# Optimization experiments

Hardware: AMD Instinct MI355X
Metric: run time of the kernel (lower is better)

Reference implementation:

```python
import jax, jax.numpy as jnp
import numpy as np

BN_EPS = 1e-5


def setup_inputs() -> dict:
    key = jax.random.key(0)
    ks = jax.random.split(key, 8)
    B, C, H, W = 8, 256, 64, 64
    Ci = 128
    x = jax.random.normal(ks[0], (B, C, H, W), dtype=jnp.float32)
    # 1x1 conv weights stored as [out, in] (kernel size 1 squeezed)
    sc = 1.0 / np.sqrt(C)
    g_w = jax.random.uniform(ks[1], (Ci, C), jnp.float32, -sc, sc)
    g_b = jax.random.uniform(ks[2], (Ci,), jnp.float32, -sc, sc)
    theta_w = jax.random.uniform(ks[3], (Ci, C), jnp.float32, -sc, sc)
    theta_b = jax.random.uniform(ks[4], (Ci,), jnp.float32, -sc, sc)
    phi_w = jax.random.uniform(ks[5], (Ci, C), jnp.float32, -sc, sc)
    phi_b = jax.random.uniform(ks[6], (Ci,), jnp.float32, -sc, sc)
    # W conv: normal(std=0.01) weight, zero bias (per _init_weights)
    W_w = 0.01 * jax.random.normal(ks[7], (C, Ci), dtype=jnp.float32)
    W_b = jnp.zeros((C,), dtype=jnp.float32)
    bn_gamma = jnp.ones((C,), dtype=jnp.float32)
    bn_beta = jnp.zeros((C,), dtype=jnp.float32)
    return {"x": x, "g_w": g_w, "g_b": g_b, "theta_w": theta_w, "theta_b": theta_b,
            "phi_w": phi_w, "phi_b": phi_b, "W_w": W_w, "W_b": W_b,
            "bn_gamma": bn_gamma, "bn_beta": bn_beta}


def reference(x, g_w, g_b, theta_w, theta_b, phi_w, phi_b, W_w, W_b, bn_gamma, bn_beta):
    B, C, H, W = x.shape
    xf = x.reshape(B, C, H * W)                                   # [B, C, N]
    # 1x1 convs == per-position channel GEMMs
    g_x = jnp.einsum('oc,bcn->bon', g_w, xf) + g_b[:, None]        # [B, Ci, N]
    th = jnp.einsum('oc,bcn->bon', theta_w, xf) + theta_b[:, None]
    ph = jnp.einsum('oc,bcn->bon', phi_w, xf) + phi_b[:, None]
    # theta^T phi : [B, N, N] dense attention scores
    f = jnp.einsum('bcn,bcm->bnm', th, ph)
    attn = jax.nn.softmax(f, axis=-1)
    # attention-weighted sum of g values -> [B, Ci, N]
    y = jnp.einsum('bnm,bcm->bcn', attn, g_x)
    # output 1x1 conv + BatchNorm2d (training-mode batch stats)
    wy = jnp.einsum('oc,bcn->bon', W_w, y) + W_b[:, None]          # [B, C, N]
    mean = jnp.mean(wy, axis=(0, 2), keepdims=True)
    var = jnp.var(wy, axis=(0, 2), keepdims=True)
    wy_bn = (wy - mean) * jax.lax.rsqrt(var + BN_EPS)
    wy_bn = wy_bn * bn_gamma[:, None] + bn_beta[:, None]
    z = wy_bn.reshape(B, C, H, W) + x
    return z
```

## Files before the change

### kernel.cpp

```cpp
#include <hip/hip_runtime.h>
#include <hip/hip_bf16.h>
#include <math.h>

#define B_   8
#define C_   256
#define CI_  128
#define N_   4096

typedef unsigned short ushort_t;
typedef unsigned int uint_t;
typedef __attribute__((ext_vector_type(8))) short short8;
typedef __attribute__((ext_vector_type(16))) float floatx16;
typedef __attribute__((ext_vector_type(2))) unsigned int uint2v;

#define OFF_W3B  0ull
#define OFF_B3   196608ull
#define OFF_WCB  198144ull
#define OFF_XT   263680ull
#define OFF_THT  17040896ull
#define OFF_PHT  25429504ull
#define OFF_G16  33818112ull
#define OFF_LP   42206720ull
#define OFF_YPB  42468864ull
#define OFF_WY   263680ull
#define OFF_ST   59246080ull

__device__ __forceinline__ ushort_t f2bf(float x) {
  union { float f; uint_t u; } c; c.f = x;
  return (ushort_t)((c.u + 0x7fffu + ((c.u >> 16) & 1u)) >> 16);
}
__device__ __forceinline__ uint_t pkbf(float a, float b) {
  __hip_bfloat162 h = __float22bfloat162_rn(float2{a, b});
  union { __hip_bfloat162 h; uint_t u; } c; c.h = h; return c.u;
}
__device__ __forceinline__ float bf_lo(uint_t u) {
  union { uint_t u; float f; } c; c.u = u << 16; return c.f;
}
__device__ __forceinline__ float bf_hi(uint_t u) {
  union { uint_t u; float f; } c; c.u = u & 0xffff0000u; return c.f;
}
__device__ __forceinline__ float fexp2(float x) {
  float r; asm("v_exp_f32 %0, %1\ns_nop 0" : "=v"(r) : "v"(x)); return r;
}
__device__ __forceinline__ void async_copy16(const void* g, void* l) {
  __builtin_amdgcn_global_load_lds(
      (const __attribute__((address_space(1))) unsigned int*)g,
      (__attribute__((address_space(3))) unsigned int*)l, 16, 0, 0);
}

__global__ __launch_bounds__(256) void pack_w(
    const float* __restrict__ g_w, const float* __restrict__ g_b,
    const float* __restrict__ th_w, const float* __restrict__ th_b,
    const float* __restrict__ ph_w, const float* __restrict__ ph_b,
    const float* __restrict__ W_w,
    ushort_t* __restrict__ W3b, float* __restrict__ b3,
    ushort_t* __restrict__ Wc)
{
  int bid = blockIdx.x;
  if (bid < 384) {
    int i = bid * 256 + threadIdx.x;
    int o = i >> 8;
    float v;
    if (o < 128)      v = g_w[i];
    else if (o < 256) v = th_w[i - 128*256];
    else              v = ph_w[i - 256*256];
    W3b[i] = f2bf(v);
    if ((i & 255) == 0)
      b3[o] = (o < 128) ? g_b[o] : (o < 256) ? th_b[o - 128] : ph_b[o - 256];
  } else {
    int j = (bid - 384) * 256 + threadIdx.x;
    Wc[j] = f2bf(W_w[j]);
  }
}

__global__ __launch_bounds__(256) void xcast(
    const float* __restrict__ x, ushort_t* __restrict__ xt)
{
  const int b = blockIdx.z, c0 = blockIdx.y * 64, n0 = blockIdx.x * 64;
  const int tid = threadIdx.x;
  __shared__ float xs[64][65];
  const int nq = (tid & 15) * 4, cr = tid >> 4;
  #pragma unroll
  for (int i = 0; i < 4; ++i) {
    float4 v = *(const float4*)&x[((size_t)b * C_ + c0 + cr + 16*i) * N_ + n0 + nq];
    xs[cr + 16*i][nq] = v.x; xs[cr + 16*i][nq+1] = v.y;
    xs[cr + 16*i][nq+2] = v.z; xs[cr + 16*i][nq+3] = v.w;
  }
  __syncthreads();
  const int n = tid >> 2, cs = (tid & 3) * 16;
  uint_t u[8];
  #pragma unroll
  for (int j = 0; j < 8; ++j)
    u[j] = pkbf(xs[cs + 2*j][n], xs[cs + 2*j + 1][n]);
  ushort_t* dst = &xt[((size_t)b * N_ + n0 + n) * C_ + c0 + cs];
  *(uint4*)dst       = make_uint4(u[0], u[1], u[2], u[3]);
  *(uint4*)(dst + 8) = make_uint4(u[4], u[5], u[6], u[7]);
}

__global__ __launch_bounds__(256, 2) void proj_all(
    const ushort_t* __restrict__ W3b, const float* __restrict__ b3,
    const ushort_t* __restrict__ xt, ushort_t* __restrict__ tht,
    ushort_t* __restrict__ pht, ushort_t* __restrict__ g16)
{
  const int b = blockIdx.z, nb = blockIdx.x, ot = blockIdx.y;
  const int gm = (ot == 2);
  const int o0 = gm ? 0 : (128 + ot * 128);
  const int tid = threadIdx.x, w = tid >> 6, lane = tid & 63;
  const int l31 = lane & 31, h = lane >> 5, xk = l31 & 7;
  __shared__ ushort_t ws_l[128 * 64];
  __shared__ ushort_t xs_l[128 * 64];
  const ushort_t* xb = xt + (size_t)b * N_ * C_;
  const int n0 = nb * 128;
  floatx16 acc[4];
  #pragma unroll
  for (int ct = 0; ct < 4; ++ct)
    #pragma unroll
    for (int r = 0; r < 16; ++r) acc[ct][r] = 0.f;

  const int gr = lane >> 3, gu = lane & 7;
  for (int k0 = 0; k0 < C_; k0 += 64) {
    __syncthreads();
    #pragma unroll
    for (int i = 0; i < 4; ++i) {
      int r = w*32 + i*8 + gr;
      async_copy16(&W3b[(size_t)(o0 + r) * C_ + k0 + ((gu ^ (r & 7)) * 8)],
                   &ws_l[(w*32 + i*8) * 64]);
      async_copy16(&xb[(size_t)(n0 + r) * C_ + k0 + ((gu ^ (r & 7)) * 8)],
                   &xs_l[(w*32 + i*8) * 64]);
    }
    __syncthreads();
    const ushort_t* bmat = gm ? ws_l : xs_l;
    const ushort_t* amat = gm ? xs_l : ws_l;
    #pragma unroll
    for (int kk = 0; kk < 4; ++kk) {
      int fc = ((2*kk + h) ^ xk) * 8;
      short8 bf = *(const short8*)&bmat[(w*32 + l31) * 64 + fc];
      #pragma unroll
      for (int ct = 0; ct < 4; ++ct) {
        short8 af = *(const short8*)&amat[(ct*32 + l31) * 64 + fc];
        acc[ct] = __builtin_amdgcn_mfma_f32_32x32x16_bf16(af, bf, acc[ct], 0, 0, 0);
      }
    }
  }

  if (gm) {
    float bv = b3[w*32 + l31];
    ushort_t* gp = g16 + ((size_t)b * CI_ + w*32 + l31) * N_;
    #pragma unroll
    for (int ct = 0; ct < 4; ++ct)
      #pragma unroll
      for (int rq = 0; rq < 4; ++rq) {
        uint2 d = make_uint2(pkbf(acc[ct][4*rq+0] + bv, acc[ct][4*rq+1] + bv),
                             pkbf(acc[ct][4*rq+2] + bv, acc[ct][4*rq+3] + bv));
        *(uint2*)&gp[n0 + ct*32 + 8*rq + 4*h] = d;
      }
  } else {
    ushort_t* tp = ((ot == 0) ? tht : pht) + ((size_t)b * N_ + n0 + w*32 + l31) * CI_;
    #pragma unroll
    for (int ct = 0; ct < 4; ++ct)
      #pragma unroll
      for (int rq = 0; rq < 4; ++rq) {
        float4 bv = *(const float4*)&b3[o0 + ct*32 + 8*rq + 4*h];
        uint2 d = make_uint2(pkbf(acc[ct][4*rq+0] + bv.x, acc[ct][4*rq+1] + bv.y),
                             pkbf(acc[ct][4*rq+2] + bv.z, acc[ct][4*rq+3] + bv.w));
        *(uint2*)&tp[ct*32 + 8*rq + 4*h] = d;
      }
  }
}

#define LOG2E_  1.442695041f
#define MBIAS_  (-28.85390082f)

__global__ __launch_bounds__(256, 3) void attn_mfma(
    const ushort_t* __restrict__ tht, const ushort_t* __restrict__ pht,
    const ushort_t* __restrict__ g16, ushort_t* __restrict__ yp,
    float* __restrict__ lp)
{
  const int b  = blockIdx.x & 7;
  const int ms = (blockIdx.x >> 3) & 1;
  const int qb = blockIdx.x >> 4;
  const int tid = threadIdx.x, w = tid >> 6, lane = tid & 63;
  const int l31 = lane & 31, h = lane >> 5, xk = l31 & 7;

  __shared__ ushort_t smem[24576];

  const int q0w = qb * 128 + w * 32;
  const int m_base = ms * 2048;

  const ushort_t* thb = tht + (size_t)b * N_ * CI_;
  const ushort_t* phb = pht + (size_t)b * N_ * CI_;
  const ushort_t* gbp = g16 + (size_t)b * CI_ * N_;

  short8 tf[8];
  #pragma unroll
  for (int kk = 0; kk < 8; ++kk)
    tf[kk] = *(const short8*)&thb[(size_t)(q0w + l31) * CI_ + kk*16 + h*8];

  floatx16 acc[4];
  #pragma unroll
  for (int ct = 0; ct < 4; ++ct)
    #pragma unroll
    for (int r = 0; r < 16; ++r) acc[ct][r] = 0.f;
  float lpart = 0.f;

  const int phr = lane >> 4, phu = lane & 15;
  const int gr  = lane >> 3, gu  = lane & 7;

  #define STAGE_PHS(m0v, bufv)                                                \
    {                                                                         \
      ushort_t* phs_ = smem + (bufv) * 8192;                                  \
      _Pragma("unroll")                                                       \
      for (int i = 0; i < 4; ++i) {                                           \
        int row = w*16 + i*4 + phr;                                           \
        async_copy16(&phb[(size_t)((m0v) + row) * CI_ + ((phu ^ (row & 7)) * 8)], \
                     &phs_[(w*16 + i*4) * 128]);                              \
      }                                                                       \
    }
  #define STAGE_GS(m0v)                                                       \
    {                                                                         \
      ushort_t* gs_ = smem + 16384;                                           \
      _Pragma("unroll")                                                       \
      for (int i = 0; i < 4; ++i) {                                           \
        int c = w*32 + i*8 + gr;                                              \
        async_copy16(&gbp[(size_t)c * N_ + (m0v) + ((gu ^ (c & 7)) * 8)],     \
                     &gs_[(w*32 + i*8) * 64]);                                \
      }                                                                       \
    }

  #define SMPV(sv, mtv)                                                       \
    {                                                                         \
      uint_t Aw[4], Bw[4];                                                    \
      float ls = 0.f;                                                         \
      _Pragma("unroll")                                                       \
      for (int rq = 0; rq < 4; ++rq) {                                        \
        float p0 = fexp2(fmaf(sv[4*rq+0], LOG2E_, MBIAS_));                   \
        float p1 = fexp2(fmaf(sv[4*rq+1], LOG2E_, MBIAS_));                   \
        float p2 = fexp2(fmaf(sv[4*rq+2], LOG2E_, MBIAS_));                   \
        float p3 = fexp2(fmaf(sv[4*rq+3], LOG2E_, MBIAS_));                   \
        ls += (p0 + p1) + (p2 + p3);                                          \
        Aw[rq] = pkbf(p0, p1);                                                \
        Bw[rq] = pkbf(p2, p3);                                                \
      }                                                                       \
      lpart += ls;                                                            \
      _Pragma("unroll")                                                       \
      for (int t = 0; t < 2; ++t) {                                           \
        uint2v ra = __builtin_amdgcn_permlane32_swap(Aw[2*t], Aw[2*t+1], false, false); \
        uint2v rb = __builtin_amdgcn_permlane32_swap(Bw[2*t], Bw[2*t+1], false, false); \
        union { uint_t u[4]; short8 s; } pk_;                                 \
        pk_.u[0] = ra.x; pk_.u[1] = rb.x; pk_.u[2] = ra.y; pk_.u[3] = rb.y;   \
        const int pc = ((2*(2*(mtv) + t) + h) ^ xk) * 8;                      \
        __builtin_amdgcn_s_setprio(1);                                        \
        _Pragma("unroll")                                                     \
        for (int ct = 0; ct < 4; ++ct) {                                      \
          short8 gf = *(const short8*)&gs[(ct*32 + l31) * 64 + pc];           \
          acc[ct] = __builtin_amdgcn_mfma_f32_32x32x16_bf16(gf, pk_.s, acc[ct], 0, 0, 0); \
        }                                                                     \
        __builtin_amdgcn_s_setprio(0);                                        \
      }                                                                       \
    }

  const ushort_t* gs = smem + 16384;

  STAGE_PHS(m_base, 0);
  asm volatile("s_waitcnt vmcnt(0)" ::: "memory");
  __builtin_amdgcn_s_barrier();

  for (int it = 0; it < 32; ++it) {
    const int cur = it & 1;
    const int m0 = m_base + it * 64;
    STAGE_GS(m0);
    if (it < 31) STAGE_PHS(m0 + 64, cur ^ 1);
    const ushort_t* phs = smem + cur * 8192;

    floatx16 s;
    #pragma unroll
    for (int r = 0; r < 16; ++r) s[r] = 0.f;
    __builtin_amdgcn_s_setprio(1);
    #pragma unroll
    for (int kk = 0; kk < 8; ++kk) {
      short8 pf = *(const short8*)&phs[l31 * 128 + (((2*kk + h) ^ xk) * 8)];
      s = __builtin_amdgcn_mfma_f32_32x32x16_bf16(pf, tf[kk], s, 0, 0, 0);
    }
    __builtin_amdgcn_s_setprio(0);

    if (it < 31) { asm volatile("s_waitcnt vmcnt(4)" ::: "memory"); }
    else         { asm volatile("s_waitcnt vmcnt(0)" ::: "memory"); }
    __builtin_amdgcn_s_barrier();

    SMPV(s, 0)

    #pragma unroll
    for (int r = 0; r < 16; ++r) s[r] = 0.f;
    __builtin_amdgcn_s_setprio(1);
    #pragma unroll
    for (int kk = 0; kk < 8; ++kk) {
      short8 pf = *(const short8*)&phs[(32 + l31) * 128 + (((2*kk + h) ^ xk) * 8)];
      s = __builtin_amdgcn_mfma_f32_32x32x16_bf16(pf, tf[kk], s, 0, 0, 0);
    }
    __builtin_amdgcn_s_setprio(0);

    SMPV(s, 1)

    asm volatile("s_waitcnt vmcnt(0)" ::: "memory");
    __builtin_amdgcn_s_barrier();
  }

  float lq = lpart + __shfl_xor(lpart, 32);
  if (h == 0)
    lp[((size_t)ms * 8 + b) * N_ + q0w + l31] = lq;

  __syncthreads();
  ushort_t* tr = smem + w * 4096;
  #pragma unroll
  for (int ct = 0; ct < 4; ++ct)
    #pragma unroll
    for (int rq = 0; rq < 4; ++rq) {
      uint2 d = make_uint2(pkbf(acc[ct][4*rq+0], acc[ct][4*rq+1]),
                           pkbf(acc[ct][4*rq+2], acc[ct][4*rq+3]));
      *(uint2*)&tr[l31 * 128 + ct*32 + 8*rq + 4*h] = d;
    }
  ushort_t* ypb = yp + (((size_t)ms * 8 + b) * N_ + q0w) * CI_;
  #pragma unroll
  for (int itx = 0; itx < 8; ++itx) {
    int row = itx*4 + (lane >> 4);
    int cu  = (lane & 15) * 8;
    uint4 v = *(const uint4*)&tr[row * 128 + cu];
    *(uint4*)&ypb[(size_t)row * CI_ + cu] = v;
  }
}

__global__ __launch_bounds__(256, 2) void wgemm_fused(
    const ushort_t* __restrict__ Wc, const float* __restrict__ Wb,
    const ushort_t* __restrict__ yp, const float* __restrict__ lp,
    ushort_t* __restrict__ WYb)
{
  const int b = blockIdx.z, nb = blockIdx.x, ot = blockIdx.y;
  const int o0 = ot * 128;
  const int tid = threadIdx.x, w = tid >> 6, lane = tid & 63;
  const int l31 = lane & 31, h = lane >> 5, xk = l31 & 7;
  __shared__ ushort_t ws_l[128 * 64];
  __shared__ ushort_t xs_l[128 * 64];
  const int n0 = nb * 128;
  const size_t PH = (size_t)B_ * N_ * CI_;
  const ushort_t* yp0 = yp + (size_t)b * N_ * CI_;
  const ushort_t* yp1 = yp0 + PH;
  floatx16 acc[4];
  #pragma unroll
  for (int ct = 0; ct < 4; ++ct)
    #pragma unroll
    for (int r = 0; r < 16; ++r) acc[ct][r] = 0.f;

  const int gr = lane >> 3, gu = lane & 7;
  for (int k0 = 0; k0 < CI_; k0 += 64) {
    __syncthreads();
    #pragma unroll
    for (int i = 0; i < 4; ++i) {
      int r = w*32 + i*8 + gr;
      async_copy16(&Wc[(size_t)(o0 + r) * CI_ + k0 + ((gu ^ (r & 7)) * 8)],
                   &ws_l[(w*32 + i*8) * 64]);
      int n = n0 + r;
      size_t src = (size_t)n * CI_ + k0 + ((gu ^ (r & 7)) * 8);
      uint4 a0 = *(const uint4*)&yp0[src];
      uint4 a1 = *(const uint4*)&yp1[src];
      float inv = 1.0f / (lp[(size_t)b * N_ + n] + lp[(size_t)(8 + b) * N_ + n]);
      uint4 o;
      o.x = pkbf((bf_lo(a0.x) + bf_lo(a1.x)) * inv, (bf_hi(a0.x) + bf_hi(a1.x)) * inv);
      o.y = pkbf((bf_lo(a0.y) + bf_lo(a1.y)) * inv, (bf_hi(a0.y) + bf_hi(a1.y)) * inv);
      o.z = pkbf((bf_lo(a0.z) + bf_lo(a1.z)) * inv, (bf_hi(a0.z) + bf_hi(a1.z)) * inv);
      o.w = pkbf((bf_lo(a0.w) + bf_lo(a1.w)) * inv, (bf_hi(a0.w) + bf_hi(a1.w)) * inv);
      *(uint4*)&xs_l[r * 64 + gu * 8] = o;
    }
    __syncthreads();
    #pragma unroll
    for (int kk = 0; kk < 4; ++kk) {
      int fc = ((2*kk + h) ^ xk) * 8;
      short8 bf = *(const short8*)&xs_l[(w*32 + l31) * 64 + fc];
      #pragma unroll
      for (int ct = 0; ct < 4; ++ct) {
        short8 af = *(const short8*)&ws_l[(ct*32 + l31) * 64 + fc];
        acc[ct] = __builtin_amdgcn_mfma_f32_32x32x16_bf16(af, bf, acc[ct], 0, 0, 0);
      }
    }
  }
  const int n = n0 + w*32 + l31;
  #pragma unroll
  for (int ct = 0; ct < 4; ++ct)
    #pragma unroll
    for (int rq = 0; rq < 4; ++rq) {
      float4 bv = *(const float4*)&Wb[o0 + ct*32 + 8*rq + 4*h];
      #pragma unroll
      for (int j = 0; j < 4; ++j) {
        int o = o0 + ct*32 + 8*rq + 4*h + j;
        WYb[((size_t)b * C_ + o) * N_ + n] = f2bf(acc[ct][4*rq + j] + (&bv.x)[j]);
      }
    }
}

__global__ __launch_bounds__(256) void bn_stats(
    const ushort_t* __restrict__ WYb, float* __restrict__ st)
{
  const int o = blockIdx.x;
  const int tid = threadIdx.x;
  float s = 0.f, s2 = 0.f;
  for (int b = 0; b < B_; ++b) {
    const ushort_t* p = WYb + ((size_t)b * C_ + o) * N_;
    for (int n = tid * 8; n < N_; n += 256 * 8) {
      uint4 v = *(const uint4*)&p[n];
      float f0 = bf_lo(v.x), f1 = bf_hi(v.x), f2 = bf_lo(v.y), f3 = bf_hi(v.y);
      float f4 = bf_lo(v.z), f5 = bf_hi(v.z), f6 = bf_lo(v.w), f7 = bf_hi(v.w);
      s  += ((f0 + f1) + (f2 + f3)) + ((f4 + f5) + (f6 + f7));
      s2 += ((f0*f0 + f1*f1) + (f2*f2 + f3*f3)) + ((f4*f4 + f5*f5) + (f6*f6 + f7*f7));
    }
  }
  __shared__ float rs[256], rs2[256];
  rs[tid] = s; rs2[tid] = s2;
  __syncthreads();
  for (int off = 128; off > 0; off >>= 1) {
    if (tid < off) { rs[tid] += rs[tid + off]; rs2[tid] += rs2[tid + off]; }
    __syncthreads();
  }
  if (tid == 0) {
    const float M = (float)(B_ * N_);
    float mean = rs[0] / M;
    float var  = rs2[0] / M - mean * mean;
    st[o] = mean;
    st[256 + o] = rsqrtf(var + 1e-5f);
  }
}

__global__ __launch_bounds__(256) void bn_apply(
    const ushort_t* __restrict__ WYb, const float* __restrict__ x,
    const float* __restrict__ st, const float* __restrict__ gamma,
    const float* __restrict__ beta, float* __restrict__ out)
{
  size_t i = ((size_t)blockIdx.x * 256 + threadIdx.x) * 4;
  int o = (int)((i >> 12) & 255);
  uint2 wv = *(const uint2*)&WYb[i];
  float4 xv = *(const float4*)&x[i];
  float gsc = gamma[o] * st[256 + o];
  float bb  = beta[o] - st[o] * gsc;
  float4 v;
  v.x = bf_lo(wv.x) * gsc + bb + xv.x;
  v.y = bf_hi(wv.x) * gsc + bb + xv.y;
  v.z = bf_lo(wv.y) * gsc + bb + xv.z;
  v.w = bf_hi(wv.y) * gsc + bb + xv.w;
  *(float4*)&out[i] = v;
}

extern "C" void kernel_launch(void* const* d_in, const int* in_sizes, int n_in,
                              void* d_out, int out_size, void* d_ws, size_t ws_size,
                              hipStream_t stream)
{
  const float* x       = (const float*)d_in[0];
  const float* g_w     = (const float*)d_in[1];
  const float* g_b     = (const float*)d_in[2];
  const float* theta_w = (const float*)d_in[3];
  const float* theta_b = (const float*)d_in[4];
  const float* phi_w   = (const float*)d_in[5];
  const float* phi_b   = (const float*)d_in[6];
  const float* W_w     = (const float*)d_in[7];
  const float* W_b     = (const float*)d_in[8];
  const float* gamma   = (const float*)d_in[9];
  const float* beta    = (const float*)d_in[10];
  float* out = (float*)d_out;

  char* ws = (char*)d_ws;
  ushort_t* W3b = (ushort_t*)(ws + OFF_W3B);
  float*    b3  = (float*)(ws + OFF_B3);
  ushort_t* Wc  = (ushort_t*)(ws + OFF_WCB);
  ushort_t* xt  = (ushort_t*)(ws + OFF_XT);
  ushort_t* tht = (ushort_t*)(ws + OFF_THT);
  ushort_t* pht = (ushort_t*)(ws + OFF_PHT);
  ushort_t* g16 = (ushort_t*)(ws + OFF_G16);
  float*    lpp = (float*)(ws + OFF_LP);
  ushort_t* ypb = (ushort_t*)(ws + OFF_YPB);
  ushort_t* WYb = (ushort_t*)(ws + OFF_WY);
  float*    ST  = (float*)(ws + OFF_ST);

  pack_w<<<512, 256, 0, stream>>>(g_w, g_b, theta_w, theta_b, phi_w, phi_b,
                                  W_w, W3b, b3, Wc);
  xcast<<<dim3(64, 4, 8), 256, 0, stream>>>(x, xt);
  proj_all<<<dim3(32, 3, 8), 256, 0, stream>>>(W3b, b3, xt, tht, pht, g16);
  attn_mfma<<<512, 256, 0, stream>>>(tht, pht, g16, ypb, lpp);
  wgemm_fused<<<dim3(32, 2, 8), 256, 0, stream>>>(Wc, W_b, ypb, lpp, WYb);
  bn_stats<<<256, 256, 0, stream>>>(WYb, ST);
  bn_apply<<<8192, 256, 0, stream>>>(WYb, x, ST, gamma, beta, out);
}
```

Baseline: 231.0 us.

## Double-buffer proj_all loads, single-stage wgemm, parallelize BN stats with atomics

proj_all now double-buffers its LDS tiles so the async load of the next K slice overlaps the MFMA work on the current one. wgemm_fused loads the whole K=128 slice in one stage, removing a barrier round. bn_stats is split across 2048 blocks that use wave shuffles and atomically add per-channel sums into a buffer that pack_w zeroes. bn_apply then derives mean and rsqrt itself. The trade-offs are more LDS per block, which can lower occupancy, and atomic float sums whose order is nondeterministic.

After: 228.4 us. About the same (-1.1%).

```diff
diff --git a/kernel.cpp b/kernel.cpp
--- a/kernel.cpp
+++ b/kernel.cpp
@@ -54,7 +54,7 @@
     const float* __restrict__ ph_w, const float* __restrict__ ph_b,
     const float* __restrict__ W_w,
     ushort_t* __restrict__ W3b, float* __restrict__ b3,
-    ushort_t* __restrict__ Wc)
+    ushort_t* __restrict__ Wc, float* __restrict__ st)
 {
   int bid = blockIdx.x;
   if (bid < 384) {
@@ -67,9 +67,12 @@
     W3b[i] = f2bf(v);
     if ((i & 255) == 0)
       b3[o] = (o < 128) ? g_b[o] : (o < 256) ? th_b[o - 128] : ph_b[o - 256];
-  } else {
+  } else if (bid < 512) {
     int j = (bid - 384) * 256 + threadIdx.x;
     Wc[j] = f2bf(W_w[j]);
+  } else {
+    st[threadIdx.x] = 0.f;
+    st[256 + threadIdx.x] = 0.f;
   }
 }
 
@@ -107,8 +110,8 @@
   const int o0 = gm ? 0 : (128 + ot * 128);
   const int tid = threadIdx.x, w = tid >> 6, lane = tid & 63;
   const int l31 = lane & 31, h = lane >> 5, xk = l31 & 7;
-  __shared__ ushort_t ws_l[128 * 64];
-  __shared__ ushort_t xs_l[128 * 64];
+  __shared__ ushort_t ws_l[2 * 128 * 64];
+  __shared__ ushort_t xs_l[2 * 128 * 64];
   const ushort_t* xb = xt + (size_t)b * N_ * C_;
   const int n0 = nb * 128;
   floatx16 acc[4];
@@ -118,19 +121,32 @@
     for (int r = 0; r < 16; ++r) acc[ct][r] = 0.f;
 
   const int gr = lane >> 3, gu = lane & 7;
-  for (int k0 = 0; k0 < C_; k0 += 64) {
-    __syncthreads();
-    #pragma unroll
-    for (int i = 0; i < 4; ++i) {
-      int r = w*32 + i*8 + gr;
-      async_copy16(&W3b[(size_t)(o0 + r) * C_ + k0 + ((gu ^ (r & 7)) * 8)],
-                   &ws_l[(w*32 + i*8) * 64]);
-      async_copy16(&xb[(size_t)(n0 + r) * C_ + k0 + ((gu ^ (r & 7)) * 8)],
-                   &xs_l[(w*32 + i*8) * 64]);
-    }
-    __syncthreads();
-    const ushort_t* bmat = gm ? ws_l : xs_l;
-    const ushort_t* amat = gm ? xs_l : ws_l;
+
+  #define PSTAGE(k0v, bufv)                                                   \
+    {                                                                         \
+      ushort_t* wsb = ws_l + (bufv) * 8192;                                   \
+      ushort_t* xsb = xs_l + (bufv) * 8192;                                   \
+      _Pragma("unroll")                                                       \
+      for (int i = 0; i < 4; ++i) {                                           \
+        int r = w*32 + i*8 + gr;                                              \
+        async_copy16(&W3b[(size_t)(o0 + r) * C_ + (k0v) + ((gu ^ (r & 7)) * 8)], \
+                     &wsb[(w*32 + i*8) * 64]);                                \
+        async_copy16(&xb[(size_t)(n0 + r) * C_ + (k0v) + ((gu ^ (r & 7)) * 8)],  \
+                     &xsb[(w*32 + i*8) * 64]);                                \
+      }                                                                       \
+    }
+
+  PSTAGE(0, 0);
+  asm volatile("s_waitcnt vmcnt(0)" ::: "memory");
+  __builtin_amdgcn_s_barrier();
+
+  for (int kt = 0; kt < 4; ++kt) {
+    const int cur = kt & 1;
+    if (kt < 3) PSTAGE((kt + 1) * 64, cur ^ 1);
+    const ushort_t* wsb = ws_l + cur * 8192;
+    const ushort_t* xsb = xs_l + cur * 8192;
+    const ushort_t* bmat = gm ? wsb : xsb;
+    const ushort_t* amat = gm ? xsb : wsb;
     #pragma unroll
     for (int kk = 0; kk < 4; ++kk) {
       int fc = ((2*kk + h) ^ xk) * 8;
@@ -141,6 +157,8 @@
         acc[ct] = __builtin_amdgcn_mfma_f32_32x32x16_bf16(af, bf, acc[ct], 0, 0, 0);
       }
     }
+    asm volatile("s_waitcnt vmcnt(0)" ::: "memory");
+    __builtin_amdgcn_s_barrier();
   }
 
   if (gm) {
@@ -338,8 +356,8 @@
   const int o0 = ot * 128;
   const int tid = threadIdx.x, w = tid >> 6, lane = tid & 63;
   const int l31 = lane & 31, h = lane >> 5, xk = l31 & 7;
-  __shared__ ushort_t ws_l[128 * 64];
-  __shared__ ushort_t xs_l[128 * 64];
+  __shared__ ushort_t ws_l[128 * 128];
+  __shared__ ushort_t xs_l[128 * 128];
   const int n0 = nb * 128;
   const size_t PH = (size_t)B_ * N_ * CI_;
   const ushort_t* yp0 = yp + (size_t)b * N_ * CI_;
@@ -350,38 +368,43 @@
     #pragma unroll
     for (int r = 0; r < 16; ++r) acc[ct][r] = 0.f;
 
-  const int gr = lane >> 3, gu = lane & 7;
-  for (int k0 = 0; k0 < CI_; k0 += 64) {
-    __syncthreads();
-    #pragma unroll
-    for (int i = 0; i < 4; ++i) {
-      int r = w*32 + i*8 + gr;
-      async_copy16(&Wc[(size_t)(o0 + r) * CI_ + k0 + ((gu ^ (r & 7)) * 8)],
-                   &ws_l[(w*32 + i*8) * 64]);
-      int n = n0 + r;
-      size_t src = (size_t)n * CI_ + k0 + ((gu ^ (r & 7)) * 8);
-      uint4 a0 = *(const uint4*)&yp0[src];
-      uint4 a1 = *(const uint4*)&yp1[src];
-      float inv = 1.0f / (lp[(size_t)b * N_ + n] + lp[(size_t)(8 + b) * N_ + n]);
-      uint4 o;
-      o.x = pkbf((bf_lo(a0.x) + bf_lo(a1.x)) * inv, (bf_hi(a0.x) + bf_hi(a1.x)) * inv);
-      o.y = pkbf((bf_lo(a0.y) + bf_lo(a1.y)) * inv, (bf_hi(a0.y) + bf_hi(a1.y)) * inv);
-      o.z = pkbf((bf_lo(a0.z) + bf_lo(a1.z)) * inv, (bf_hi(a0.z) + bf_hi(a1.z)) * inv);
-      o.w = pkbf((bf_lo(a0.w) + bf_lo(a1.w)) * inv, (bf_hi(a0.w) + bf_hi(a1.w)) * inv);
-      *(uint4*)&xs_l[r * 64 + gu * 8] = o;
-    }
-    __syncthreads();
-    #pragma unroll
-    for (int kk = 0; kk < 4; ++kk) {
-      int fc = ((2*kk + h) ^ xk) * 8;
-      short8 bf = *(const short8*)&xs_l[(w*32 + l31) * 64 + fc];
-      #pragma unroll
-      for (int ct = 0; ct < 4; ++ct) {
-        short8 af = *(const short8*)&ws_l[(ct*32 + l31) * 64 + fc];
-        acc[ct] = __builtin_amdgcn_mfma_f32_32x32x16_bf16(af, bf, acc[ct], 0, 0, 0);
-      }
-    }
-  }
+  const int rr = lane >> 4;
+  const int uu = lane & 15;
+
+  #pragma unroll
+  for (int i = 0; i < 8; ++i) {
+    int r = w*32 + i*4 + rr;
+    async_copy16(&Wc[(size_t)(o0 + r) * CI_ + ((uu ^ (r & 7)) * 8)],
+                 &ws_l[(w*32 + i*4) * 128]);
+  }
+  #pragma unroll
+  for (int i = 0; i < 8; ++i) {
+    int rl = w*32 + i*4 + rr;
+    int n = n0 + rl;
+    size_t src = (size_t)n * CI_ + ((uu ^ (rl & 7)) * 8);
+    uint4 a0 = *(const uint4*)&yp0[src];
+    uint4 a1 = *(const uint4*)&yp1[src];
+    float inv = 1.0f / (lp[(size_t)b * N_ + n] + lp[(size_t)(8 + b) * N_ + n]);
+    uint4 o;
+    o.x = pkbf((bf_lo(a0.x) + bf_lo(a1.x)) * inv, (bf_hi(a0.x) + bf_hi(a1.x)) * inv);
+    o.y = pkbf((bf_lo(a0.y) + bf_lo(a1.y)) * inv, (bf_hi(a0.y) + bf_hi(a1.y)) * inv);
+    o.z = pkbf((bf_lo(a0.z) + bf_lo(a1.z)) * inv, (bf_hi(a0.z) + bf_hi(a1.z)) * inv);
+    o.w = pkbf((bf_lo(a0.w) + bf_lo(a1.w)) * inv, (bf_hi(a0.w) + bf_hi(a1.w)) * inv);
+    *(uint4*)&xs_l[rl * 128 + uu * 8] = o;
+  }
+  __syncthreads();
+
+  #pragma unroll
+  for (int kk = 0; kk < 8; ++kk) {
+    int fc = ((2*kk + h) ^ xk) * 8;
+    short8 bf = *(const short8*)&xs_l[(w*32 + l31) * 128 + fc];
+    #pragma unroll
+    for (int ct = 0; ct < 4; ++ct) {
+      short8 af = *(const short8*)&ws_l[(ct*32 + l31) * 128 + fc];
+      acc[ct] = __builtin_amdgcn_mfma_f32_32x32x16_bf16(af, bf, acc[ct], 0, 0, 0);
+    }
+  }
+
   const int n = n0 + w*32 + l31;
   #pragma unroll
   for (int ct = 0; ct < 4; ++ct)
@@ -399,32 +422,31 @@
 __global__ __launch_bounds__(256) void bn_stats(
     const ushort_t* __restrict__ WYb, float* __restrict__ st)
 {
-  const int o = blockIdx.x;
+  const int o  = blockIdx.x & 255;
+  const int bb = blockIdx.x >> 8;
   const int tid = threadIdx.x;
+  const ushort_t* p = WYb + ((size_t)bb * C_ + o) * N_;
   float s = 0.f, s2 = 0.f;
-  for (int b = 0; b < B_; ++b) {
-    const ushort_t* p = WYb + ((size_t)b * C_ + o) * N_;
-    for (int n = tid * 8; n < N_; n += 256 * 8) {
-      uint4 v = *(const uint4*)&p[n];
-      float f0 = bf_lo(v.x), f1 = bf_hi(v.x), f2 = bf_lo(v.y), f3 = bf_hi(v.y);
-      float f4 = bf_lo(v.z), f5 = bf_hi(v.z), f6 = bf_lo(v.w), f7 = bf_hi(v.w);
-      s  += ((f0 + f1) + (f2 + f3)) + ((f4 + f5) + (f6 + f7));
-      s2 += ((f0*f0 + f1*f1) + (f2*f2 + f3*f3)) + ((f4*f4 + f5*f5) + (f6*f6 + f7*f7));
-    }
-  }
-  __shared__ float rs[256], rs2[256];
-  rs[tid] = s; rs2[tid] = s2;
+  #pragma unroll
+  for (int j = 0; j < 2; ++j) {
+    uint4 v = *(const uint4*)&p[tid * 16 + j * 8];
+    float f0 = bf_lo(v.x), f1 = bf_hi(v.x), f2 = bf_lo(v.y), f3 = bf_hi(v.y);
+    float f4 = bf_lo(v.z), f5 = bf_hi(v.z), f6 = bf_lo(v.w), f7 = bf_hi(v.w);
+    s  += ((f0 + f1) + (f2 + f3)) + ((f4 + f5) + (f6 + f7));
+    s2 += ((f0*f0 + f1*f1) + (f2*f2 + f3*f3)) + ((f4*f4 + f5*f5) + (f6*f6 + f7*f7));
+  }
+  #pragma unroll
+  for (int m = 32; m >= 1; m >>= 1) {
+    s  += __shfl_xor(s, m);
+    s2 += __shfl_xor(s2, m);
+  }
+  __shared__ float rs[8];
+  const int w = tid >> 6, lane = tid & 63;
+  if (lane == 0) { rs[w] = s; rs[4 + w] = s2; }
   __syncthreads();
-  for (int off = 128; off > 0; off >>= 1) {
-    if (tid < off) { rs[tid] += rs[tid + off]; rs2[tid] += rs2[tid + off]; }
-    __syncthreads();
-  }
   if (tid == 0) {
-    const float M = (float)(B_ * N_);
-    float mean = rs[0] / M;
-    float var  = rs2[0] / M - mean * mean;
-    st[o] = mean;
-    st[256 + o] = rsqrtf(var + 1e-5f);
+    atomicAdd(&st[o],       (rs[0] + rs[1]) + (rs[2] + rs[3]));
+    atomicAdd(&st[256 + o], (rs[4] + rs[5]) + (rs[6] + rs[7]));
   }
 }
 
@@ -437,8 +459,11 @@
   int o = (int)((i >> 12) & 255);
   uint2 wv = *(const uint2*)&WYb[i];
   float4 xv = *(const float4*)&x[i];
-  float gsc = gamma[o] * st[256 + o];
-  float bb  = beta[o] - st[o] * gsc;
+  const float invM = 1.0f / (float)(B_ * N_);
+  float mean = st[o] * invM;
+  float var  = st[256 + o] * invM - mean * mean;
+  float gsc = gamma[o] * rsqrtf(var + 1e-5f);
+  float bb  = beta[o] - mean * gsc;
   float4 v;
   v.x = bf_lo(wv.x) * gsc + bb + xv.x;
   v.y = bf_hi(wv.x) * gsc + bb + xv.y;
@@ -477,12 +502,12 @@
   ushort_t* WYb = (ushort_t*)(ws + OFF_WY);
   float*    ST  = (float*)(ws + OFF_ST);
 
-  pack_w<<<512, 256, 0, stream>>>(g_w, g_b, theta_w, theta_b, phi_w, phi_b,
-                                  W_w, W3b, b3, Wc);
+  pack_w<<<513, 256, 0, stream>>>(g_w, g_b, theta_w, theta_b, phi_w, phi_b,
+                                  W_w, W3b, b3, Wc, ST);
   xcast<<<dim3(64, 4, 8), 256, 0, stream>>>(x, xt);
   proj_all<<<dim3(32, 3, 8), 256, 0, stream>>>(W3b, b3, xt, tht, pht, g16);
   attn_mfma<<<512, 256, 0, stream>>>(tht, pht, g16, ypb, lpp);
   wgemm_fused<<<dim3(32, 2, 8), 256, 0, stream>>>(Wc, W_b, ypb, lpp, WYb);
-  bn_stats<<<256, 256, 0, stream>>>(WYb, ST);
+  bn_stats<<<2048, 256, 0, stream>>>(WYb, ST);
   bn_apply<<<8192, 256, 0, stream>>>(WYb, x, ST, gamma, beta, out);
 }
```
